# Kernel tuning notes

Hardware: AMD Instinct MI355X
Metric: run time of the kernel (lower is better)

## Reference

```python
import jax, jax.numpy as jnp
import numpy as np

B, P, C = 64, 196, 768   # batch, num_patches, hidden_size
HS = 384                 # hidden_s (token-mixing hidden dim)
NG = 8                   # num_grids
GMIN, GMAX = -1.0, 1.0


def _rbf(x):
    # fast-KAN radial basis: exp(-((x - grid_i)/denom)^2), grid over [GMIN, GMAX]
    grid = jnp.linspace(GMIN, GMAX, NG).astype(x.dtype)
    denom = (GMAX - GMIN) / (NG - 1)
    return jnp.exp(-jnp.square((x[..., None] - grid) / denom))  # [..., din, NG]


def _kan_linear(x, spline_w, base_w, base_b):
    # x: [..., din]; spline_w: [dout, din*NG]; base_w: [dout, din]; base_b: [dout]
    basis = _rbf(x).reshape(*x.shape[:-1], -1)          # [..., din*NG]
    out = basis @ spline_w.T                            # spline term (no bias)
    out = out + jax.nn.silu(x) @ base_w.T + base_b      # base update term
    return out


def setup_inputs() -> dict:
    key = jax.random.key(0)
    ks = jax.random.split(key, 5)
    s = 0.1  # spline_weight_init_scale
    return {
        "x": jax.random.normal(ks[0], (B, P, C), jnp.float32),
        "fc1_spline_w": jax.random.normal(ks[1], (HS, P * NG), jnp.float32) * (s / np.sqrt(P * NG)),
        "fc1_base_w": jax.random.normal(ks[2], (HS, P), jnp.float32) / np.sqrt(P),
        "fc1_base_b": jnp.zeros((HS,), jnp.float32),
        "fc2_spline_w": jax.random.normal(ks[3], (P, HS * NG), jnp.float32) * (s / np.sqrt(HS * NG)),
        "fc2_base_w": jax.random.normal(ks[4], (P, HS), jnp.float32) / np.sqrt(HS),
        "fc2_base_b": jnp.zeros((P,), jnp.float32),
    }


def reference(x, fc1_spline_w, fc1_base_w, fc1_base_b,
              fc2_spline_w, fc2_base_w, fc2_base_b):
    skip_param = 1.0
    # token mixing: permute so KANLinear acts over the patch axis
    h = jnp.swapaxes(x, 1, 2)                                   # [B, C, P]
    h = _kan_linear(h, fc1_spline_w, fc1_base_w, fc1_base_b)    # [B, C, HS]
    # dropout p=0 -> identity; the two intermediate permutes cancel
    h = _kan_linear(h, fc2_spline_w, fc2_base_w, fc2_base_b)    # [B, C, P]
    out = jnp.swapaxes(h, 1, 2)                                 # [B, P, C]
    return out + skip_param * x
```

## Files before the change

### kernel.cpp

```cpp
#include <hip/hip_runtime.h>
#include <cstdint>

#define B_  64
#define P_  196
#define C_  768
#define HS_ 384
#define M_  49152
#define RT_ 96
#define NB_ (M_ / RT_)

#define NC1 13
#define KT1 111
#define NT1 12
#define NC2 24
#define KT2 216
#define NT2 7

#define H1_ELEMS  ((size_t)M_ * HS_)
#define W1P_ELEMS ((size_t)KT1 * NT1 * 512)
#define W2P_ELEMS ((size_t)KT2 * NT2 * 512)

typedef __attribute__((ext_vector_type(8)))  short short8;
typedef __attribute__((ext_vector_type(16))) float f32x16;

#define MFMA(w, a, c) __builtin_amdgcn_mfma_f32_32x32x16_bf16((w), (a), (c), 0, 0, 0)

static __device__ __forceinline__ float bf2f(unsigned short u) {
    union { unsigned int i; float f; } v; v.i = ((unsigned int)u) << 16; return v.f;
}
static __device__ __forceinline__ unsigned short f2bf_rne(float f) {
    union { float f; unsigned int i; } v; v.f = f;
    unsigned int r = v.i + 0x7FFFu + ((v.i >> 16) & 1u);
    return (unsigned short)(r >> 16);
}
static __device__ __forceinline__ unsigned int pack2(float a, float b) {
    unsigned int ua = __float_as_uint(a) + 0x8000u;
    unsigned int ub = __float_as_uint(b) + 0x8000u;
    return __builtin_amdgcn_perm(ub, ua, 0x07060302u);
}
static __device__ __forceinline__ short8 rbf8(float s) {
    const float Rr = 1.2011224087864498f;
    const float Aa = 4.2039284307525743f;
    float t1 = __builtin_fmaf(Aa, s, Aa);
    union { short8 s8; unsigned int u[4]; } r;
#pragma unroll
    for (int q = 0; q < 4; q++) {
        float u0 = t1 - (float)(2 * q) * Rr;
        float u1 = t1 - (float)(2 * q + 1) * Rr;
        r.u[q] = pack2(__builtin_amdgcn_exp2f(-u0 * u0),
                       __builtin_amdgcn_exp2f(-u1 * u1));
    }
    return r.s8;
}
static __device__ __forceinline__ unsigned int silu2(float a, float b) {
    const float L2E = 1.4426950408889634f;
    float fa = a * __builtin_amdgcn_rcpf(1.f + __builtin_amdgcn_exp2f(-L2E * a));
    float fb = b * __builtin_amdgcn_rcpf(1.f + __builtin_amdgcn_exp2f(-L2E * b));
    return pack2(fa, fb);
}

static __device__ __forceinline__ void block_sync_lds() {
    __builtin_amdgcn_sched_barrier(0);
    asm volatile("s_waitcnt lgkmcnt(0)" ::: "memory");
    __builtin_amdgcn_s_barrier();
    __builtin_amdgcn_sched_barrier(0);
}

__global__ void pack_w_kernel(const float* __restrict__ w1s,
                              const float* __restrict__ w1b,
                              const float* __restrict__ w2s,
                              const float* __restrict__ w2b,
                              unsigned short* __restrict__ w1p,
                              unsigned short* __restrict__ w2p) {
    size_t idx = (size_t)blockIdx.x * 256 + threadIdx.x;
    if (idx < W1P_ELEMS) {
        int j    = idx & 7;
        int lane = (idx >> 3) & 63;
        int lin  = idx >> 9;
        int nt   = lin % NT1;
        int tt   = lin / NT1;
        int cc   = (tt < 108) ? tt / 9 : 12;
        int kk   = (tt < 108) ? tt % 9 : (tt - 108);
        int ktl  = (cc < 12) ? kk : ((kk < 2) ? kk : 8);
        int n = nt * 32 + (lane & 31);
        int khalf = lane >> 5;
        float v = 0.f;
        if (ktl < 8) {
            int p = cc * 16 + ktl * 2 + khalf;
            if (p < P_) v = w1s[(size_t)n * 1568 + p * 8 + j];
        } else {
            int p = cc * 16 + khalf * 8 + j;
            if (p < P_) v = w1b[(size_t)n * 196 + p];
        }
        w1p[idx] = f2bf_rne(v);
    } else {
        size_t idx2 = idx - W1P_ELEMS;
        if (idx2 < W2P_ELEMS) {
            int j    = idx2 & 7;
            int lane = (idx2 >> 3) & 63;
            int lin  = idx2 >> 9;
            int nt   = lin % NT2;
            int tt   = lin / NT2;
            int cc   = tt / 9;
            int ktl  = tt % 9;
            int n = nt * 32 + (lane & 31);
            int khalf = lane >> 5;
            float v = 0.f;
            if (n < P_) {
                if (ktl < 8) {
                    int s = cc * 16 + ktl * 2 + khalf;
                    v = w2s[(size_t)n * 3072 + s * 8 + j];
                } else {
                    int s = cc * 16 + khalf * 8 + j;
                    v = w2b[(size_t)n * 384 + s];
                }
            }
            w2p[idx2] = f2bf_rne(v);
        }
    }
}

#define TS_  1536
#define FB_  (9 * TS_)


__global__ __launch_bounds__(256, 2)
void fc1_kernel(const float* __restrict__ x,
                const unsigned short* __restrict__ w1p,
                const float* __restrict__ b1,
                unsigned short* __restrict__ h1t) {
    __shared__ __align__(16) unsigned short frag[2 * FB_];
    int blk = blockIdx.x;
    int tid = threadIdx.x;
    int b   = blk >> 3;
    int c0  = (blk & 7) * RT_;
    const float* xb = x + (size_t)b * (P_ * C_);

    int colA = tid & 63, scA = tid >> 6;
    int colB = 64 + (tid & 31), scB = tid >> 5;
    int pbase_rbfA  = ((colA >> 5) << 9) + (colA & 31) * 8;
    int pbase_rbfB  = 1024 + (colB & 31) * 8;
    int pbase_siluA = 8 * TS_ + ((colA >> 5) << 9) + ((scA >> 1) << 8) + (colA & 31) * 8 + (scA & 1) * 4;
    int pbase_siluB = 8 * TS_ + 1024 + ((scB >> 2) << 8) + (colB & 31) * 8 + (scB & 3) * 2;

    int wave = tid >> 6, lane = tid & 63;
    int l31 = lane & 31, half = lane >> 5;
    int nt0 = wave * 3;

    f32x16 acc[3][3];
#pragma unroll
    for (int rt = 0; rt < 3; rt++)
#pragma unroll
        for (int nt = 0; nt < 3; nt++)
#pragma unroll
            for (int i = 0; i < 16; i++) acc[rt][nt][i] = 0.f;

    const short8* wp = (const short8*)w1p;
    short8 wbuf[2][3];

    auto wload = [&](int d, const short8* wt0, int kk) {
        const short8* wt = wt0 + (size_t)kk * (NT1 * 64);
        wbuf[d][0] = wt[0]; wbuf[d][1] = wt[64]; wbuf[d][2] = wt[128];
    };
    auto do_mfma = [&](short8 w0, short8 w1, short8 w2,
                       short8 a0, short8 a1, short8 a2) {
        acc[0][0] = MFMA(w0, a0, acc[0][0]); acc[1][0] = MFMA(w0, a1, acc[1][0]); acc[2][0] = MFMA(w0, a2, acc[2][0]);
        acc[0][1] = MFMA(w1, a0, acc[0][1]); acc[1][1] = MFMA(w1, a1, acc[1][1]); acc[2][1] = MFMA(w1, a2, acc[2][1]);
        acc[0][2] = MFMA(w2, a0, acc[0][2]); acc[1][2] = MFMA(w2, a1, acc[1][2]); acc[2][2] = MFMA(w2, a2, acc[2][2]);
    };
    auto produce = [&](int fb, const float (&ra)[4], const float (&rb2)[2]) {
#pragma unroll
        for (int i = 0; i < 4; i++) {
            int sl = scA * 4 + i;
            *(short8*)&frag[fb + (sl >> 1) * TS_ + ((sl & 1) << 8) + pbase_rbfA] = rbf8(ra[i]);
        }
#pragma unroll
        for (int i = 0; i < 2; i++) {
            int sl = scB * 2 + i;
            *(short8*)&frag[fb + (sl >> 1) * TS_ + ((sl & 1) << 8) + pbase_rbfB] = rbf8(rb2[i]);
        }
        uint2 sv;
        sv.x = silu2(ra[0], ra[1]);
        sv.y = silu2(ra[2], ra[3]);
        *(uint2*)&frag[fb + pbase_siluA] = sv;
        *(unsigned int*)&frag[fb + pbase_siluB] = silu2(rb2[0], rb2[1]);
    };
    auto body = [&](int cc, const float (&rbPA)[4], const float (&rbPB)[2],
                    float (&rbLA)[4], float (&rbLB)[2]) {
        const short8* wt0 = wp + ((size_t)(cc * 9) * NT1 + nt0) * 64 + lane;
        wload(0, wt0, 0); wload(1, wt0, 1);
        int fbP = ((cc + 1) & 1) * FB_;
        const unsigned short* fg = &frag[(cc & 1) * FB_];
        short8 a0 = *(const short8*)&fg[lane * 8];
        short8 a1 = *(const short8*)&fg[512 + lane * 8];
        short8 a2 = *(const short8*)&fg[1024 + lane * 8];
#pragma unroll
        for (int kk = 0; kk < 9; kk++) {
            short8 na0, na1, na2;
            if (kk < 8) {
                na0 = *(const short8*)&fg[(kk + 1) * TS_ + lane * 8];
                na1 = *(const short8*)&fg[(kk + 1) * TS_ + 512 + lane * 8];
                na2 = *(const short8*)&fg[(kk + 1) * TS_ + 1024 + lane * 8];
            }
            short8 w0 = wbuf[kk & 1][0], w1 = wbuf[kk & 1][1], w2 = wbuf[kk & 1][2];
            if (kk < 7) wload(kk & 1, wt0, kk + 2);
            if (kk < 4) {
                int sl = scA * 4 + kk;
                *(short8*)&frag[fbP + (sl >> 1) * TS_ + ((sl & 1) << 8) + pbase_rbfA] = rbf8(rbPA[kk]);
            } else if (kk == 4) {
#pragma unroll
                for (int i = 0; i < 2; i++) {
                    int sl = scB * 2 + i;
                    *(short8*)&frag[fbP + (sl >> 1) * TS_ + ((sl & 1) << 8) + pbase_rbfB] = rbf8(rbPB[i]);
                }
            } else if (kk == 5) {
                uint2 sv;
                sv.x = silu2(rbPA[0], rbPA[1]);
                sv.y = silu2(rbPA[2], rbPA[3]);
                *(uint2*)&frag[fbP + pbase_siluA] = sv;
                *(unsigned int*)&frag[fbP + pbase_siluB] = silu2(rbPB[0], rbPB[1]);
            } else if (kk == 6) {
#pragma unroll
                for (int i = 0; i < 2; i++) {
                    int p = (cc + 2) * 16 + scA * 4 + i;
                    p = (p < P_) ? p : (P_ - 1);
                    rbLA[i] = xb[(size_t)p * C_ + c0 + colA];
                }
            } else if (kk == 7) {
#pragma unroll
                for (int i = 2; i < 4; i++) {
                    int p = (cc + 2) * 16 + scA * 4 + i;
                    p = (p < P_) ? p : (P_ - 1);
                    rbLA[i] = xb[(size_t)p * C_ + c0 + colA];
                }
            } else {
#pragma unroll
                for (int i = 0; i < 2; i++) {
                    int p = (cc + 2) * 16 + scB * 2 + i;
                    p = (p < P_) ? p : (P_ - 1);
                    rbLB[i] = xb[(size_t)p * C_ + c0 + colB];
                }
            }
            do_mfma(w0, w1, w2, a0, a1, a2);
            if (kk < 8) { a0 = na0; a1 = na1; a2 = na2; }
        }
        block_sync_lds();
    };

    float rbA_A[4], rbB_A[4], rbA_B[2], rbB_B[2];
#pragma unroll
    for (int i = 0; i < 4; i++) {
        rbA_A[i] = xb[(size_t)(scA * 4 + i) * C_ + c0 + colA];
        rbB_A[i] = xb[(size_t)(16 + scA * 4 + i) * C_ + c0 + colA];
    }
#pragma unroll
    for (int i = 0; i < 2; i++) {
        rbA_B[i] = xb[(size_t)(scB * 2 + i) * C_ + c0 + colB];
        rbB_B[i] = xb[(size_t)(16 + scB * 2 + i) * C_ + c0 + colB];
    }
    produce(0, rbA_A, rbA_B);
    block_sync_lds();

    for (int c2 = 0; c2 < 6; c2++) {
        body(2 * c2,     rbB_A, rbB_B, rbA_A, rbA_B);
        body(2 * c2 + 1, rbA_A, rbA_B, rbB_A, rbB_B);
    }
    {
        const short8* wt0 = wp + ((size_t)108 * NT1 + nt0) * 64 + lane;
        wload(0, wt0, 0); wload(1, wt0, 1);
        const unsigned short* fg = &frag[0];
#pragma unroll
        for (int kk = 0; kk < 3; kk++) {
            short8 w0 = wbuf[kk & 1][0], w1 = wbuf[kk & 1][1], w2 = wbuf[kk & 1][2];
            if (kk == 0) wload(0, wt0, 2);
            int ktl = (kk < 2) ? kk : 8;
            short8 a0 = *(const short8*)&fg[ktl * TS_ + lane * 8];
            short8 a1 = *(const short8*)&fg[ktl * TS_ + 512 + lane * 8];
            short8 a2 = *(const short8*)&fg[ktl * TS_ + 1024 + lane * 8];
            do_mfma(w0, w1, w2, a0, a1, a2);
        }
    }

#pragma unroll
    for (int nt = 0; nt < 3; nt++) {
        int n0 = (nt0 + nt) * 32 + 4 * half;
#pragma unroll
        for (int reg = 0; reg < 16; reg++) {
            int n = n0 + (reg & 3) + 8 * (reg >> 2);
            float bv = b1[n];
#pragma unroll
            for (int rt = 0; rt < 3; rt++) {
                h1t[(size_t)n * M_ + blk * RT_ + rt * 32 + l31] = f2bf_rne(acc[rt][nt][reg] + bv);
            }
        }
    }
}

__global__ __launch_bounds__(256, 2)
void fc2_kernel(const unsigned short* __restrict__ h1t,
                const unsigned short* __restrict__ w2p,
                const float* __restrict__ b2,
                const float* __restrict__ x,
                float* __restrict__ out) {
    __shared__ __align__(16) unsigned short frag[2 * FB_];
    int blk = blockIdx.x;
    int tid = threadIdx.x;
    int rbase = blk * RT_;

    int colA = tid & 63, scA = tid >> 6;
    int colB = 64 + (tid & 31), scB = tid >> 5;
    int pbase_rbfA  = ((colA >> 5) << 9) + (colA & 31) * 8;
    int pbase_rbfB  = 1024 + (colB & 31) * 8;
    int pbase_siluA = 8 * TS_ + ((colA >> 5) << 9) + ((scA >> 1) << 8) + (colA & 31) * 8 + (scA & 1) * 4;
    int pbase_siluB = 8 * TS_ + 1024 + ((scB >> 2) << 8) + (colB & 31) * 8 + (scB & 3) * 2;

    int wave = tid >> 6, lane = tid & 63;
    int l31 = lane & 31, half = lane >> 5;
    int nt0 = wave * 2;
    int ntn = (wave < 3) ? 2 : 1;
    int off1 = (ntn > 1) ? 64 : 0;

    f32x16 acc[3][2];
#pragma unroll
    for (int rt = 0; rt < 3; rt++)
#pragma unroll
        for (int nt = 0; nt < 2; nt++)
#pragma unroll
            for (int i = 0; i < 16; i++) acc[rt][nt][i] = 0.f;

    const short8* wp = (const short8*)w2p;
    short8 wbuf[2][2];

    auto wload = [&](int d, const short8* wt0, int kk) {
        const short8* wt = wt0 + (size_t)kk * (NT2 * 64);
        wbuf[d][0] = wt[0]; wbuf[d][1] = wt[off1];
    };
    auto do_mfma = [&](short8 w0, short8 w1, short8 a0, short8 a1, short8 a2) {
        acc[0][0] = MFMA(w0, a0, acc[0][0]); acc[1][0] = MFMA(w0, a1, acc[1][0]); acc[2][0] = MFMA(w0, a2, acc[2][0]);
        if (ntn == 2) {
            acc[0][1] = MFMA(w1, a0, acc[0][1]); acc[1][1] = MFMA(w1, a1, acc[1][1]); acc[2][1] = MFMA(w1, a2, acc[2][1]);
        }
    };
    auto produce = [&](int fb, const unsigned short (&ra)[4], const unsigned short (&rb2)[2]) {
        float v0 = bf2f(ra[0]), v1 = bf2f(ra[1]), v2 = bf2f(ra[2]), v3 = bf2f(ra[3]);
        float u0 = bf2f(rb2[0]), u1 = bf2f(rb2[1]);
        float vv[4] = {v0, v1, v2, v3};
#pragma unroll
        for (int i = 0; i < 4; i++) {
            int sl = scA * 4 + i;
            *(short8*)&frag[fb + (sl >> 1) * TS_ + ((sl & 1) << 8) + pbase_rbfA] = rbf8(vv[i]);
        }
        float uu[2] = {u0, u1};
#pragma unroll
        for (int i = 0; i < 2; i++) {
            int sl = scB * 2 + i;
            *(short8*)&frag[fb + (sl >> 1) * TS_ + ((sl & 1) << 8) + pbase_rbfB] = rbf8(uu[i]);
        }
        uint2 sv;
        sv.x = silu2(v0, v1);
        sv.y = silu2(v2, v3);
        *(uint2*)&frag[fb + pbase_siluA] = sv;
        *(unsigned int*)&frag[fb + pbase_siluB] = silu2(u0, u1);
    };
    auto body = [&](int cc, const unsigned short (&rbPA)[4], const unsigned short (&rbPB)[2],
                    unsigned short (&rbLA)[4], unsigned short (&rbLB)[2]) {
        bool doProd = (cc + 1 < NC2);
        const short8* wt0 = wp + ((size_t)(cc * 9) * NT2 + nt0) * 64 + lane;
        wload(0, wt0, 0); wload(1, wt0, 1);
        int fbP = ((cc + 1) & 1) * FB_;
        const unsigned short* fg = &frag[(cc & 1) * FB_];
        short8 a0 = *(const short8*)&fg[lane * 8];
        short8 a1 = *(const short8*)&fg[512 + lane * 8];
        short8 a2 = *(const short8*)&fg[1024 + lane * 8];
#pragma unroll
        for (int kk = 0; kk < 9; kk++) {
            short8 na0, na1, na2;
            if (kk < 8) {
                na0 = *(const short8*)&fg[(kk + 1) * TS_ + lane * 8];
                na1 = *(const short8*)&fg[(kk + 1) * TS_ + 512 + lane * 8];
                na2 = *(const short8*)&fg[(kk + 1) * TS_ + 1024 + lane * 8];
            }
            short8 w0 = wbuf[kk & 1][0], w1 = wbuf[kk & 1][1];
            if (kk < 7) wload(kk & 1, wt0, kk + 2);
            if (kk < 4) {
                if (doProd) {
                    int sl = scA * 4 + kk;
                    *(short8*)&frag[fbP + (sl >> 1) * TS_ + ((sl & 1) << 8) + pbase_rbfA] =
                        rbf8(bf2f(rbPA[kk]));
                }
            } else if (kk == 4) {
                if (doProd) {
#pragma unroll
                    for (int i = 0; i < 2; i++) {
                        int sl = scB * 2 + i;
                        *(short8*)&frag[fbP + (sl >> 1) * TS_ + ((sl & 1) << 8) + pbase_rbfB] =
                            rbf8(bf2f(rbPB[i]));
                    }
                }
            } else if (kk == 5) {
                if (doProd) {
                    uint2 sv;
                    sv.x = silu2(bf2f(rbPA[0]), bf2f(rbPA[1]));
                    sv.y = silu2(bf2f(rbPA[2]), bf2f(rbPA[3]));
                    *(uint2*)&frag[fbP + pbase_siluA] = sv;
                    *(unsigned int*)&frag[fbP + pbase_siluB] = silu2(bf2f(rbPB[0]), bf2f(rbPB[1]));
                }
            } else if (kk == 6) {
#pragma unroll
                for (int i = 0; i < 2; i++) {
                    int s = (cc + 2) * 16 + scA * 4 + i;
                    s = (s < HS_) ? s : (HS_ - 1);
                    rbLA[i] = h1t[(size_t)s * M_ + rbase + colA];
                }
            } else if (kk == 7) {
#pragma unroll
                for (int i = 2; i < 4; i++) {
                    int s = (cc + 2) * 16 + scA * 4 + i;
                    s = (s < HS_) ? s : (HS_ - 1);
                    rbLA[i] = h1t[(size_t)s * M_ + rbase + colA];
                }
            } else {
#pragma unroll
                for (int i = 0; i < 2; i++) {
                    int s = (cc + 2) * 16 + scB * 2 + i;
                    s = (s < HS_) ? s : (HS_ - 1);
                    rbLB[i] = h1t[(size_t)s * M_ + rbase + colB];
                }
            }
            do_mfma(w0, w1, a0, a1, a2);
            if (kk < 8) { a0 = na0; a1 = na1; a2 = na2; }
        }
        block_sync_lds();
    };

    unsigned short rbA_A[4], rbB_A[4], rbA_B[2], rbB_B[2];
#pragma unroll
    for (int i = 0; i < 4; i++) {
        rbA_A[i] = h1t[(size_t)(scA * 4 + i) * M_ + rbase + colA];
        rbB_A[i] = h1t[(size_t)(16 + scA * 4 + i) * M_ + rbase + colA];
    }
#pragma unroll
    for (int i = 0; i < 2; i++) {
        rbA_B[i] = h1t[(size_t)(scB * 2 + i) * M_ + rbase + colB];
        rbB_B[i] = h1t[(size_t)(16 + scB * 2 + i) * M_ + rbase + colB];
    }
    produce(0, rbA_A, rbA_B);
    block_sync_lds();

    for (int c2 = 0; c2 < 12; c2++) {
        body(2 * c2,     rbB_A, rbB_B, rbA_A, rbA_B);
        body(2 * c2 + 1, rbA_A, rbA_B, rbB_A, rbB_B);
    }

    int b = blk >> 3;
    int c0 = (blk & 7) * RT_;
#pragma unroll
    for (int nt = 0; nt < 2; nt++) {
        if (nt < ntn) {
            int p0 = (nt0 + nt) * 32 + 4 * half;
#pragma unroll
            for (int reg = 0; reg < 16; reg++) {
                int p = p0 + (reg & 3) + 8 * (reg >> 2);
                if (p < P_) {
                    float bv = b2[p];
#pragma unroll
                    for (int rt = 0; rt < 3; rt++) {
                        size_t off = ((size_t)b * P_ + p) * C_ + c0 + rt * 32 + l31;
                        out[off] = acc[rt][nt][reg] + bv + x[off];
                    }
                }
            }
        }
    }
}

extern "C" void kernel_launch(void* const* d_in, const int* in_sizes, int n_in,
                              void* d_out, int out_size, void* d_ws, size_t ws_size,
                              hipStream_t stream) {
    const float* x   = (const float*)d_in[0];
    const float* w1s = (const float*)d_in[1];
    const float* w1b = (const float*)d_in[2];
    const float* b1  = (const float*)d_in[3];
    const float* w2s = (const float*)d_in[4];
    const float* w2b = (const float*)d_in[5];
    const float* b2  = (const float*)d_in[6];
    float* out = (float*)d_out;

    unsigned short* h1t = (unsigned short*)d_ws;
    unsigned short* w1p = h1t + H1_ELEMS;
    unsigned short* w2p = w1p + W1P_ELEMS;

    int pack_blocks = (int)((W1P_ELEMS + W2P_ELEMS) / 256);
    pack_w_kernel<<<pack_blocks, 256, 0, stream>>>(w1s, w1b, w2s, w2b, w1p, w2p);
    fc1_kernel<<<NB_, 256, 0, stream>>>(x, w1p, b1, h1t);
    fc2_kernel<<<NB_, 256, 0, stream>>>(h1t, w2p, b2, x, out);
}
```

Before: 243.4 us.

## Warp-specialize fc1/fc2 into producer waves and MFMA consumer waves

Both GEMM kernels now launch 512 threads. Four producer waves load inputs and compute RBF and SiLU fragments into a 4-deep LDS ring, and four consumer waves, raised in priority, only load weights and issue MFMAs. This moves basis computation and global loads out of the MFMA loop so they overlap with matrix work. In exchange, LDS use doubles and occupancy drops to one block per CU, with one block-wide barrier per pair of chunks.

```diff
diff --git a/kernel.cpp b/kernel.cpp
--- a/kernel.cpp
+++ b/kernel.cpp
@@ -123,27 +123,78 @@
 #define TS_  1536
 #define FB_  (9 * TS_)
 
-
-__global__ __launch_bounds__(256, 2)
+__global__ __launch_bounds__(512, 1)
 void fc1_kernel(const float* __restrict__ x,
                 const unsigned short* __restrict__ w1p,
                 const float* __restrict__ b1,
                 unsigned short* __restrict__ h1t) {
-    __shared__ __align__(16) unsigned short frag[2 * FB_];
+    __shared__ __align__(16) unsigned short frag[4 * FB_];
     int blk = blockIdx.x;
     int tid = threadIdx.x;
     int b   = blk >> 3;
     int c0  = (blk & 7) * RT_;
     const float* xb = x + (size_t)b * (P_ * C_);
-
-    int colA = tid & 63, scA = tid >> 6;
-    int colB = 64 + (tid & 31), scB = tid >> 5;
-    int pbase_rbfA  = ((colA >> 5) << 9) + (colA & 31) * 8;
-    int pbase_rbfB  = 1024 + (colB & 31) * 8;
-    int pbase_siluA = 8 * TS_ + ((colA >> 5) << 9) + ((scA >> 1) << 8) + (colA & 31) * 8 + (scA & 1) * 4;
-    int pbase_siluB = 8 * TS_ + 1024 + ((scB >> 2) << 8) + (colB & 31) * 8 + (scB & 3) * 2;
-
-    int wave = tid >> 6, lane = tid & 63;
+    int wave = tid >> 6;
+
+    if (wave >= 4) {
+        int ptid = tid & 255;
+        int colA = ptid & 63, scA = ptid >> 6;
+        int colB = 64 + (ptid & 31), scB = ptid >> 5;
+        int pbase_rbfA  = ((colA >> 5) << 9) + (colA & 31) * 8;
+        int pbase_rbfB  = 1024 + (colB & 31) * 8;
+        int pbase_siluA = 8 * TS_ + ((colA >> 5) << 9) + ((scA >> 1) << 8) + (colA & 31) * 8 + (scA & 1) * 4;
+        int pbase_siluB = 8 * TS_ + 1024 + ((scB >> 2) << 8) + (colB & 31) * 8 + (scB & 3) * 2;
+
+        auto loadc = [&](int cc, float (&va)[4], float (&vb)[2]) {
+#pragma unroll
+            for (int i = 0; i < 4; i++) {
+                int p = cc * 16 + scA * 4 + i; p = (p < P_) ? p : (P_ - 1);
+                va[i] = xb[(size_t)p * C_ + c0 + colA];
+            }
+#pragma unroll
+            for (int i = 0; i < 2; i++) {
+                int p = cc * 16 + scB * 2 + i; p = (p < P_) ? p : (P_ - 1);
+                vb[i] = xb[(size_t)p * C_ + c0 + colB];
+            }
+        };
+        auto produce = [&](int cc, const float (&ra)[4], const float (&rb2)[2]) {
+            int fb = (cc & 3) * FB_;
+#pragma unroll
+            for (int i = 0; i < 4; i++) {
+                int sl = scA * 4 + i;
+                *(short8*)&frag[fb + (sl >> 1) * TS_ + ((sl & 1) << 8) + pbase_rbfA] = rbf8(ra[i]);
+            }
+#pragma unroll
+            for (int i = 0; i < 2; i++) {
+                int sl = scB * 2 + i;
+                *(short8*)&frag[fb + (sl >> 1) * TS_ + ((sl & 1) << 8) + pbase_rbfB] = rbf8(rb2[i]);
+            }
+            uint2 sv;
+            sv.x = silu2(ra[0], ra[1]);
+            sv.y = silu2(ra[2], ra[3]);
+            *(uint2*)&frag[fb + pbase_siluA] = sv;
+            *(unsigned int*)&frag[fb + pbase_siluB] = silu2(rb2[0], rb2[1]);
+        };
+
+        float vA[4], uA[2], vB[4], uB[2];
+        loadc(0, vA, uA); loadc(1, vB, uB);
+        produce(0, vA, uA); produce(1, vB, uB);
+        loadc(2, vA, uA); loadc(3, vB, uB);
+        block_sync_lds();
+        for (int t = 0; t < 7; t++) {
+            int cP = 2 * t + 2;
+            if (cP     < NC1) produce(cP,     vA, uA);
+            if (cP + 1 < NC1) produce(cP + 1, vB, uB);
+            int n0 = (cP + 2 < NC1) ? cP + 2 : NC1 - 1;
+            int n1 = (cP + 3 < NC1) ? cP + 3 : NC1 - 1;
+            loadc(n0, vA, uA); loadc(n1, vB, uB);
+            block_sync_lds();
+        }
+        return;
+    }
+
+    __builtin_amdgcn_s_setprio(1);
+    int lane = tid & 63;
     int l31 = lane & 31, half = lane >> 5;
     int nt0 = wave * 3;
 
@@ -158,6 +209,7 @@
     const short8* wp = (const short8*)w1p;
     short8 wbuf[2][3];
 
+    auto wt0_of = [&](int cc) { return wp + ((size_t)(cc * 9) * NT1 + nt0) * 64 + lane; };
     auto wload = [&](int d, const short8* wt0, int kk) {
         const short8* wt = wt0 + (size_t)kk * (NT1 * 64);
         wbuf[d][0] = wt[0]; wbuf[d][1] = wt[64]; wbuf[d][2] = wt[128];
@@ -168,29 +220,8 @@
         acc[0][1] = MFMA(w1, a0, acc[0][1]); acc[1][1] = MFMA(w1, a1, acc[1][1]); acc[2][1] = MFMA(w1, a2, acc[2][1]);
         acc[0][2] = MFMA(w2, a0, acc[0][2]); acc[1][2] = MFMA(w2, a1, acc[1][2]); acc[2][2] = MFMA(w2, a2, acc[2][2]);
     };
-    auto produce = [&](int fb, const float (&ra)[4], const float (&rb2)[2]) {
-#pragma unroll
-        for (int i = 0; i < 4; i++) {
-            int sl = scA * 4 + i;
-            *(short8*)&frag[fb + (sl >> 1) * TS_ + ((sl & 1) << 8) + pbase_rbfA] = rbf8(ra[i]);
-        }
-#pragma unroll
-        for (int i = 0; i < 2; i++) {
-            int sl = scB * 2 + i;
-            *(short8*)&frag[fb + (sl >> 1) * TS_ + ((sl & 1) << 8) + pbase_rbfB] = rbf8(rb2[i]);
-        }
-        uint2 sv;
-        sv.x = silu2(ra[0], ra[1]);
-        sv.y = silu2(ra[2], ra[3]);
-        *(uint2*)&frag[fb + pbase_siluA] = sv;
-        *(unsigned int*)&frag[fb + pbase_siluB] = silu2(rb2[0], rb2[1]);
-    };
-    auto body = [&](int cc, const float (&rbPA)[4], const float (&rbPB)[2],
-                    float (&rbLA)[4], float (&rbLB)[2]) {
-        const short8* wt0 = wp + ((size_t)(cc * 9) * NT1 + nt0) * 64 + lane;
-        wload(0, wt0, 0); wload(1, wt0, 1);
-        int fbP = ((cc + 1) & 1) * FB_;
-        const unsigned short* fg = &frag[(cc & 1) * FB_];
+    auto consume = [&](int cc, const short8* wt0) {
+        const unsigned short* fg = &frag[(cc & 3) * FB_];
         short8 a0 = *(const short8*)&fg[lane * 8];
         short8 a1 = *(const short8*)&fg[512 + lane * 8];
         short8 a2 = *(const short8*)&fg[1024 + lane * 8];
@@ -204,81 +235,39 @@
             }
             short8 w0 = wbuf[kk & 1][0], w1 = wbuf[kk & 1][1], w2 = wbuf[kk & 1][2];
             if (kk < 7) wload(kk & 1, wt0, kk + 2);
-            if (kk < 4) {
-                int sl = scA * 4 + kk;
-                *(short8*)&frag[fbP + (sl >> 1) * TS_ + ((sl & 1) << 8) + pbase_rbfA] = rbf8(rbPA[kk]);
-            } else if (kk == 4) {
-#pragma unroll
-                for (int i = 0; i < 2; i++) {
-                    int sl = scB * 2 + i;
-                    *(short8*)&frag[fbP + (sl >> 1) * TS_ + ((sl & 1) << 8) + pbase_rbfB] = rbf8(rbPB[i]);
-                }
-            } else if (kk == 5) {
-                uint2 sv;
-                sv.x = silu2(rbPA[0], rbPA[1]);
-                sv.y = silu2(rbPA[2], rbPA[3]);
-                *(uint2*)&frag[fbP + pbase_siluA] = sv;
-                *(unsigned int*)&frag[fbP + pbase_siluB] = silu2(rbPB[0], rbPB[1]);
-            } else if (kk == 6) {
-#pragma unroll
-                for (int i = 0; i < 2; i++) {
-                    int p = (cc + 2) * 16 + scA * 4 + i;
-                    p = (p < P_) ? p : (P_ - 1);
-                    rbLA[i] = xb[(size_t)p * C_ + c0 + colA];
-                }
-            } else if (kk == 7) {
-#pragma unroll
-                for (int i = 2; i < 4; i++) {
-                    int p = (cc + 2) * 16 + scA * 4 + i;
-                    p = (p < P_) ? p : (P_ - 1);
-                    rbLA[i] = xb[(size_t)p * C_ + c0 + colA];
-                }
-            } else {
-#pragma unroll
-                for (int i = 0; i < 2; i++) {
-                    int p = (cc + 2) * 16 + scB * 2 + i;
-                    p = (p < P_) ? p : (P_ - 1);
-                    rbLB[i] = xb[(size_t)p * C_ + c0 + colB];
-                }
-            }
             do_mfma(w0, w1, w2, a0, a1, a2);
             if (kk < 8) { a0 = na0; a1 = na1; a2 = na2; }
         }
+    };
+
+    const short8* wtP = wt0_of(0);
+    wload(0, wtP, 0); wload(1, wtP, 1);
+    block_sync_lds();
+    for (int t = 0; t < 7; t++) {
+        if (t < 6) {
+            consume(2 * t, wtP);
+            const short8* wtQ = wt0_of(2 * t + 1);
+            wload(0, wtQ, 0); wload(1, wtQ, 1);
+            consume(2 * t + 1, wtQ);
+            wtP = wt0_of(2 * t + 2);
+            wload(0, wtP, 0); wload(1, wtP, 1);
+        } else {
+            const unsigned short* fg = &frag[(12 & 3) * FB_];
+            short8 a0 = *(const short8*)&fg[lane * 8];
+            short8 a1 = *(const short8*)&fg[512 + lane * 8];
+            short8 a2 = *(const short8*)&fg[1024 + lane * 8];
+            short8 c0v = *(const short8*)&fg[TS_ + lane * 8];
+            short8 c1v = *(const short8*)&fg[TS_ + 512 + lane * 8];
+            short8 c2v = *(const short8*)&fg[TS_ + 1024 + lane * 8];
+            short8 s0 = *(const short8*)&fg[8 * TS_ + lane * 8];
+            short8 s1 = *(const short8*)&fg[8 * TS_ + 512 + lane * 8];
+            short8 s2 = *(const short8*)&fg[8 * TS_ + 1024 + lane * 8];
+            do_mfma(wbuf[0][0], wbuf[0][1], wbuf[0][2], a0, a1, a2);
+            wload(0, wtP, 2);
+            do_mfma(wbuf[1][0], wbuf[1][1], wbuf[1][2], c0v, c1v, c2v);
+            do_mfma(wbuf[0][0], wbuf[0][1], wbuf[0][2], s0, s1, s2);
+        }
         block_sync_lds();
-    };
-
-    float rbA_A[4], rbB_A[4], rbA_B[2], rbB_B[2];
-#pragma unroll
-    for (int i = 0; i < 4; i++) {
-        rbA_A[i] = xb[(size_t)(scA * 4 + i) * C_ + c0 + colA];
-        rbB_A[i] = xb[(size_t)(16 + scA * 4 + i) * C_ + c0 + colA];
-    }
-#pragma unroll
-    for (int i = 0; i < 2; i++) {
-        rbA_B[i] = xb[(size_t)(scB * 2 + i) * C_ + c0 + colB];
-        rbB_B[i] = xb[(size_t)(16 + scB * 2 + i) * C_ + c0 + colB];
-    }
-    produce(0, rbA_A, rbA_B);
-    block_sync_lds();
-
-    for (int c2 = 0; c2 < 6; c2++) {
-        body(2 * c2,     rbB_A, rbB_B, rbA_A, rbA_B);
-        body(2 * c2 + 1, rbA_A, rbA_B, rbB_A, rbB_B);
-    }
-    {
-        const short8* wt0 = wp + ((size_t)108 * NT1 + nt0) * 64 + lane;
-        wload(0, wt0, 0); wload(1, wt0, 1);
-        const unsigned short* fg = &frag[0];
-#pragma unroll
-        for (int kk = 0; kk < 3; kk++) {
-            short8 w0 = wbuf[kk & 1][0], w1 = wbuf[kk & 1][1], w2 = wbuf[kk & 1][2];
-            if (kk == 0) wload(0, wt0, 2);
-            int ktl = (kk < 2) ? kk : 8;
-            short8 a0 = *(const short8*)&fg[ktl * TS_ + lane * 8];
-            short8 a1 = *(const short8*)&fg[ktl * TS_ + 512 + lane * 8];
-            short8 a2 = *(const short8*)&fg[ktl * TS_ + 1024 + lane * 8];
-            do_mfma(w0, w1, w2, a0, a1, a2);
-        }
     }
 
 #pragma unroll
@@ -296,25 +285,81 @@
     }
 }
 
-__global__ __launch_bounds__(256, 2)
+__global__ __launch_bounds__(512, 1)
 void fc2_kernel(const unsigned short* __restrict__ h1t,
                 const unsigned short* __restrict__ w2p,
                 const float* __restrict__ b2,
                 const float* __restrict__ x,
                 float* __restrict__ out) {
-    __shared__ __align__(16) unsigned short frag[2 * FB_];
+    __shared__ __align__(16) unsigned short frag[4 * FB_];
     int blk = blockIdx.x;
     int tid = threadIdx.x;
     int rbase = blk * RT_;
-
-    int colA = tid & 63, scA = tid >> 6;
-    int colB = 64 + (tid & 31), scB = tid >> 5;
-    int pbase_rbfA  = ((colA >> 5) << 9) + (colA & 31) * 8;
-    int pbase_rbfB  = 1024 + (colB & 31) * 8;
-    int pbase_siluA = 8 * TS_ + ((colA >> 5) << 9) + ((scA >> 1) << 8) + (colA & 31) * 8 + (scA & 1) * 4;
-    int pbase_siluB = 8 * TS_ + 1024 + ((scB >> 2) << 8) + (colB & 31) * 8 + (scB & 3) * 2;
-
-    int wave = tid >> 6, lane = tid & 63;
+    int wave = tid >> 6;
+
+    if (wave >= 4) {
+        int ptid = tid & 255;
+        int colA = ptid & 63, scA = ptid >> 6;
+        int colB = 64 + (ptid & 31), scB = ptid >> 5;
+        int pbase_rbfA  = ((colA >> 5) << 9) + (colA & 31) * 8;
+        int pbase_rbfB  = 1024 + (colB & 31) * 8;
+        int pbase_siluA = 8 * TS_ + ((colA >> 5) << 9) + ((scA >> 1) << 8) + (colA & 31) * 8 + (scA & 1) * 4;
+        int pbase_siluB = 8 * TS_ + 1024 + ((scB >> 2) << 8) + (colB & 31) * 8 + (scB & 3) * 2;
+
+        auto loadc = [&](int cc, unsigned short (&va)[4], unsigned short (&vb)[2]) {
+#pragma unroll
+            for (int i = 0; i < 4; i++) {
+                int s = cc * 16 + scA * 4 + i; s = (s < HS_) ? s : (HS_ - 1);
+                va[i] = h1t[(size_t)s * M_ + rbase + colA];
+            }
+#pragma unroll
+            for (int i = 0; i < 2; i++) {
+                int s = cc * 16 + scB * 2 + i; s = (s < HS_) ? s : (HS_ - 1);
+                vb[i] = h1t[(size_t)s * M_ + rbase + colB];
+            }
+        };
+        auto produce = [&](int cc, const unsigned short (&ra)[4], const unsigned short (&rb2)[2]) {
+            int fb = (cc & 3) * FB_;
+            float v0 = bf2f(ra[0]), v1 = bf2f(ra[1]), v2 = bf2f(ra[2]), v3 = bf2f(ra[3]);
+            float u0 = bf2f(rb2[0]), u1 = bf2f(rb2[1]);
+            float vv[4] = {v0, v1, v2, v3};
+#pragma unroll
+            for (int i = 0; i < 4; i++) {
+                int sl = scA * 4 + i;
+                *(short8*)&frag[fb + (sl >> 1) * TS_ + ((sl & 1) << 8) + pbase_rbfA] = rbf8(vv[i]);
+            }
+            float uu[2] = {u0, u1};
+#pragma unroll
+            for (int i = 0; i < 2; i++) {
+                int sl = scB * 2 + i;
+                *(short8*)&frag[fb + (sl >> 1) * TS_ + ((sl & 1) << 8) + pbase_rbfB] = rbf8(uu[i]);
+            }
+            uint2 sv;
+            sv.x = silu2(v0, v1);
+            sv.y = silu2(v2, v3);
+            *(uint2*)&frag[fb + pbase_siluA] = sv;
+            *(unsigned int*)&frag[fb + pbase_siluB] = silu2(u0, u1);
+        };
+
+        unsigned short vA[4], uA[2], vB[4], uB[2];
+        loadc(0, vA, uA); loadc(1, vB, uB);
+        produce(0, vA, uA); produce(1, vB, uB);
+        loadc(2, vA, uA); loadc(3, vB, uB);
+        block_sync_lds();
+        for (int t = 0; t < 12; t++) {
+            int cP = 2 * t + 2;
+            if (cP     < NC2) produce(cP,     vA, uA);
+            if (cP + 1 < NC2) produce(cP + 1, vB, uB);
+            int n0 = (cP + 2 < NC2) ? cP + 2 : NC2 - 1;
+            int n1 = (cP + 3 < NC2) ? cP + 3 : NC2 - 1;
+            loadc(n0, vA, uA); loadc(n1, vB, uB);
+            block_sync_lds();
+        }
+        return;
+    }
+
+    __builtin_amdgcn_s_setprio(1);
+    int lane = tid & 63;
     int l31 = lane & 31, half = lane >> 5;
     int nt0 = wave * 2;
     int ntn = (wave < 3) ? 2 : 1;
@@ -331,6 +376,7 @@
     const short8* wp = (const short8*)w2p;
     short8 wbuf[2][2];
 
+    auto wt0_of = [&](int cc) { return wp + ((size_t)(cc * 9) * NT2 + nt0) * 64 + lane; };
     auto wload = [&](int d, const short8* wt0, int kk) {
         const short8* wt = wt0 + (size_t)kk * (NT2 * 64);
         wbuf[d][0] = wt[0]; wbuf[d][1] = wt[off1];
@@ -341,34 +387,8 @@
             acc[0][1] = MFMA(w1, a0, acc[0][1]); acc[1][1] = MFMA(w1, a1, acc[1][1]); acc[2][1] = MFMA(w1, a2, acc[2][1]);
         }
     };
-    auto produce = [&](int fb, const unsigned short (&ra)[4], const unsigned short (&rb2)[2]) {
-        float v0 = bf2f(ra[0]), v1 = bf2f(ra[1]), v2 = bf2f(ra[2]), v3 = bf2f(ra[3]);
-        float u0 = bf2f(rb2[0]), u1 = bf2f(rb2[1]);
-        float vv[4] = {v0, v1, v2, v3};
-#pragma unroll
-        for (int i = 0; i < 4; i++) {
-            int sl = scA * 4 + i;
-            *(short8*)&frag[fb + (sl >> 1) * TS_ + ((sl & 1) << 8) + pbase_rbfA] = rbf8(vv[i]);
-        }
-        float uu[2] = {u0, u1};
-#pragma unroll
-        for (int i = 0; i < 2; i++) {
-            int sl = scB * 2 + i;
-            *(short8*)&frag[fb + (sl >> 1) * TS_ + ((sl & 1) << 8) + pbase_rbfB] = rbf8(uu[i]);
-        }
-        uint2 sv;
-        sv.x = silu2(v0, v1);
-        sv.y = silu2(v2, v3);
-        *(uint2*)&frag[fb + pbase_siluA] = sv;
-        *(unsigned int*)&frag[fb + pbase_siluB] = silu2(u0, u1);
-    };
-    auto body = [&](int cc, const unsigned short (&rbPA)[4], const unsigned short (&rbPB)[2],
-                    unsigned short (&rbLA)[4], unsigned short (&rbLB)[2]) {
-        bool doProd = (cc + 1 < NC2);
-        const short8* wt0 = wp + ((size_t)(cc * 9) * NT2 + nt0) * 64 + lane;
-        wload(0, wt0, 0); wload(1, wt0, 1);
-        int fbP = ((cc + 1) & 1) * FB_;
-        const unsigned short* fg = &frag[(cc & 1) * FB_];
+    auto consume = [&](int cc, const short8* wt0) {
+        const unsigned short* fg = &frag[(cc & 3) * FB_];
         short8 a0 = *(const short8*)&fg[lane * 8];
         short8 a1 = *(const short8*)&fg[512 + lane * 8];
         short8 a2 = *(const short8*)&fg[1024 + lane * 8];
@@ -382,74 +402,23 @@
             }
             short8 w0 = wbuf[kk & 1][0], w1 = wbuf[kk & 1][1];
             if (kk < 7) wload(kk & 1, wt0, kk + 2);
-            if (kk < 4) {
-                if (doProd) {
-                    int sl = scA * 4 + kk;
-                    *(short8*)&frag[fbP + (sl >> 1) * TS_ + ((sl & 1) << 8) + pbase_rbfA] =
-                        rbf8(bf2f(rbPA[kk]));
-                }
-            } else if (kk == 4) {
-                if (doProd) {
-#pragma unroll
-                    for (int i = 0; i < 2; i++) {
-                        int sl = scB * 2 + i;
-                        *(short8*)&frag[fbP + (sl >> 1) * TS_ + ((sl & 1) << 8) + pbase_rbfB] =
-                            rbf8(bf2f(rbPB[i]));
-                    }
-                }
-            } else if (kk == 5) {
-                if (doProd) {
-                    uint2 sv;
-                    sv.x = silu2(bf2f(rbPA[0]), bf2f(rbPA[1]));
-                    sv.y = silu2(bf2f(rbPA[2]), bf2f(rbPA[3]));
-                    *(uint2*)&frag[fbP + pbase_siluA] = sv;
-                    *(unsigned int*)&frag[fbP + pbase_siluB] = silu2(bf2f(rbPB[0]), bf2f(rbPB[1]));
-                }
-            } else if (kk == 6) {
-#pragma unroll
-                for (int i = 0; i < 2; i++) {
-                    int s = (cc + 2) * 16 + scA * 4 + i;
-                    s = (s < HS_) ? s : (HS_ - 1);
-                    rbLA[i] = h1t[(size_t)s * M_ + rbase + colA];
-                }
-            } else if (kk == 7) {
-#pragma unroll
-                for (int i = 2; i < 4; i++) {
-                    int s = (cc + 2) * 16 + scA * 4 + i;
-                    s = (s < HS_) ? s : (HS_ - 1);
-                    rbLA[i] = h1t[(size_t)s * M_ + rbase + colA];
-                }
-            } else {
-#pragma unroll
-                for (int i = 0; i < 2; i++) {
-                    int s = (cc + 2) * 16 + scB * 2 + i;
-                    s = (s < HS_) ? s : (HS_ - 1);
-                    rbLB[i] = h1t[(size_t)s * M_ + rbase + colB];
-                }
-            }
             do_mfma(w0, w1, a0, a1, a2);
             if (kk < 8) { a0 = na0; a1 = na1; a2 = na2; }
         }
+    };
+
+    const short8* wtP = wt0_of(0);
+    wload(0, wtP, 0); wload(1, wtP, 1);
+    block_sync_lds();
+    for (int t = 0; t < 12; t++) {
+        consume(2 * t, wtP);
+        const short8* wtQ = wt0_of(2 * t + 1);
+        wload(0, wtQ, 0); wload(1, wtQ, 1);
+        consume(2 * t + 1, wtQ);
+        int nc = (2 * t + 2 < NC2) ? 2 * t + 2 : NC2 - 1;
+        wtP = wt0_of(nc);
+        wload(0, wtP, 0); wload(1, wtP, 1);
         block_sync_lds();
-    };
-
-    unsigned short rbA_A[4], rbB_A[4], rbA_B[2], rbB_B[2];
-#pragma unroll
-    for (int i = 0; i < 4; i++) {
-        rbA_A[i] = h1t[(size_t)(scA * 4 + i) * M_ + rbase + colA];
-        rbB_A[i] = h1t[(size_t)(16 + scA * 4 + i) * M_ + rbase + colA];
-    }
-#pragma unroll
-    for (int i = 0; i < 2; i++) {
-        rbA_B[i] = h1t[(size_t)(scB * 2 + i) * M_ + rbase + colB];
-        rbB_B[i] = h1t[(size_t)(16 + scB * 2 + i) * M_ + rbase + colB];
-    }
-    produce(0, rbA_A, rbA_B);
-    block_sync_lds();
-
-    for (int c2 = 0; c2 < 12; c2++) {
-        body(2 * c2,     rbB_A, rbB_B, rbA_A, rbA_B);
-        body(2 * c2 + 1, rbA_A, rbA_B, rbB_A, rbB_B);
     }
 
     int b = blk >> 3;
@@ -492,6 +461,6 @@
 
     int pack_blocks = (int)((W1P_ELEMS + W2P_ELEMS) / 256);
     pack_w_kernel<<<pack_blocks, 256, 0, stream>>>(w1s, w1b, w2s, w2b, w1p, w2p);
-    fc1_kernel<<<NB_, 256, 0, stream>>>(x, w1p, b1, h1t);
-    fc2_kernel<<<NB_, 256, 0, stream>>>(h1t, w2p, b2, x, out);
-}
+    fc1_kernel<<<NB_, 512, 0, stream>>>(x, w1p, b1, h1t);
+    fc2_kernel<<<NB_, 512, 0, stream>>>(h1t, w2p, b2, x, out);
+}
```

Measured after the change: 291.2 us. 1.2x slower.

## Restructure fc2 inner loop into three phases with batched loads and setprio MFMA bursts

Applied to the files above, without the earlier changes.

Replaces the per-k software-pipelined loop in the fc2 kernel (next fragment and weight prefetched one step ahead) with three phases per chunk. Each phase first loads three k-steps of A fragments from LDS and weights from global, does its share of producer and global-load work, then runs a block barrier and a burst of MFMAs under raised wave priority. The intent is to group memory and compute so waves on a CU interleave MFMA bursts better. In exchange it adds three barriers per chunk instead of one, removes the one-step-ahead register prefetch so global weight-load latency is exposed before each burst, and raises register pressure from the larger fragment and weight buffers.

```diff
diff --git a/kernel.cpp b/kernel.cpp
--- a/kernel.cpp
+++ b/kernel.cpp
@@ -123,7 +123,6 @@
 #define TS_  1536
 #define FB_  (9 * TS_)
 
-
 __global__ __launch_bounds__(256, 2)
 void fc1_kernel(const float* __restrict__ x,
                 const unsigned short* __restrict__ w1p,
@@ -329,18 +328,9 @@
             for (int i = 0; i < 16; i++) acc[rt][nt][i] = 0.f;
 
     const short8* wp = (const short8*)w2p;
-    short8 wbuf[2][2];
-
-    auto wload = [&](int d, const short8* wt0, int kk) {
-        const short8* wt = wt0 + (size_t)kk * (NT2 * 64);
-        wbuf[d][0] = wt[0]; wbuf[d][1] = wt[off1];
-    };
-    auto do_mfma = [&](short8 w0, short8 w1, short8 a0, short8 a1, short8 a2) {
-        acc[0][0] = MFMA(w0, a0, acc[0][0]); acc[1][0] = MFMA(w0, a1, acc[1][0]); acc[2][0] = MFMA(w0, a2, acc[2][0]);
-        if (ntn == 2) {
-            acc[0][1] = MFMA(w1, a0, acc[0][1]); acc[1][1] = MFMA(w1, a1, acc[1][1]); acc[2][1] = MFMA(w1, a2, acc[2][1]);
-        }
-    };
+    short8 wbuf[3][2];
+    short8 af[3][3];
+
     auto produce = [&](int fb, const unsigned short (&ra)[4], const unsigned short (&rb2)[2]) {
         float v0 = bf2f(ra[0]), v1 = bf2f(ra[1]), v2 = bf2f(ra[2]), v3 = bf2f(ra[3]);
         float u0 = bf2f(rb2[0]), u1 = bf2f(rb2[1]);
@@ -362,33 +352,56 @@
         *(uint2*)&frag[fb + pbase_siluA] = sv;
         *(unsigned int*)&frag[fb + pbase_siluB] = silu2(u0, u1);
     };
+
     auto body = [&](int cc, const unsigned short (&rbPA)[4], const unsigned short (&rbPB)[2],
                     unsigned short (&rbLA)[4], unsigned short (&rbLB)[2]) {
         bool doProd = (cc + 1 < NC2);
-        const short8* wt0 = wp + ((size_t)(cc * 9) * NT2 + nt0) * 64 + lane;
-        wload(0, wt0, 0); wload(1, wt0, 1);
+        const unsigned short* fg = &frag[(cc & 1) * FB_];
         int fbP = ((cc + 1) & 1) * FB_;
-        const unsigned short* fg = &frag[(cc & 1) * FB_];
-        short8 a0 = *(const short8*)&fg[lane * 8];
-        short8 a1 = *(const short8*)&fg[512 + lane * 8];
-        short8 a2 = *(const short8*)&fg[1024 + lane * 8];
-#pragma unroll
-        for (int kk = 0; kk < 9; kk++) {
-            short8 na0, na1, na2;
-            if (kk < 8) {
-                na0 = *(const short8*)&fg[(kk + 1) * TS_ + lane * 8];
-                na1 = *(const short8*)&fg[(kk + 1) * TS_ + 512 + lane * 8];
-                na2 = *(const short8*)&fg[(kk + 1) * TS_ + 1024 + lane * 8];
-            }
-            short8 w0 = wbuf[kk & 1][0], w1 = wbuf[kk & 1][1];
-            if (kk < 7) wload(kk & 1, wt0, kk + 2);
-            if (kk < 4) {
+#pragma unroll
+        for (int p = 0; p < 3; p++) {
+#pragma unroll
+            for (int k = 0; k < 3; k++) {
+                int t = 3 * p + k;
+                af[k][0] = *(const short8*)&fg[t * TS_ + lane * 8];
+                af[k][1] = *(const short8*)&fg[t * TS_ + 512 + lane * 8];
+                af[k][2] = *(const short8*)&fg[t * TS_ + 1024 + lane * 8];
+            }
+            const short8* wt0 = wp + ((size_t)(cc * 9 + 3 * p) * NT2 + nt0) * 64 + lane;
+#pragma unroll
+            for (int k = 0; k < 3; k++) {
+                const short8* wt = wt0 + (size_t)k * (NT2 * 64);
+                wbuf[k][0] = wt[0]; wbuf[k][1] = wt[off1];
+            }
+            if (p == 0) {
                 if (doProd) {
-                    int sl = scA * 4 + kk;
-                    *(short8*)&frag[fbP + (sl >> 1) * TS_ + ((sl & 1) << 8) + pbase_rbfA] =
-                        rbf8(bf2f(rbPA[kk]));
-                }
-            } else if (kk == 4) {
+#pragma unroll
+                    for (int i = 0; i < 2; i++) {
+                        int sl = scA * 4 + i;
+                        *(short8*)&frag[fbP + (sl >> 1) * TS_ + ((sl & 1) << 8) + pbase_rbfA] =
+                            rbf8(bf2f(rbPA[i]));
+                    }
+                }
+#pragma unroll
+                for (int i = 0; i < 2; i++) {
+                    int s = (cc + 2) * 16 + scA * 4 + i; s = (s < HS_) ? s : (HS_ - 1);
+                    rbLA[i] = h1t[(size_t)s * M_ + rbase + colA];
+                }
+            } else if (p == 1) {
+                if (doProd) {
+#pragma unroll
+                    for (int i = 2; i < 4; i++) {
+                        int sl = scA * 4 + i;
+                        *(short8*)&frag[fbP + (sl >> 1) * TS_ + ((sl & 1) << 8) + pbase_rbfA] =
+                            rbf8(bf2f(rbPA[i]));
+                    }
+                }
+#pragma unroll
+                for (int i = 2; i < 4; i++) {
+                    int s = (cc + 2) * 16 + scA * 4 + i; s = (s < HS_) ? s : (HS_ - 1);
+                    rbLA[i] = h1t[(size_t)s * M_ + rbase + colA];
+                }
+            } else {
                 if (doProd) {
 #pragma unroll
                     for (int i = 0; i < 2; i++) {
@@ -396,41 +409,34 @@
                         *(short8*)&frag[fbP + (sl >> 1) * TS_ + ((sl & 1) << 8) + pbase_rbfB] =
                             rbf8(bf2f(rbPB[i]));
                     }
-                }
-            } else if (kk == 5) {
-                if (doProd) {
                     uint2 sv;
                     sv.x = silu2(bf2f(rbPA[0]), bf2f(rbPA[1]));
                     sv.y = silu2(bf2f(rbPA[2]), bf2f(rbPA[3]));
                     *(uint2*)&frag[fbP + pbase_siluA] = sv;
                     *(unsigned int*)&frag[fbP + pbase_siluB] = silu2(bf2f(rbPB[0]), bf2f(rbPB[1]));
                 }
-            } else if (kk == 6) {
 #pragma unroll
                 for (int i = 0; i < 2; i++) {
-                    int s = (cc + 2) * 16 + scA * 4 + i;
-                    s = (s < HS_) ? s : (HS_ - 1);
-                    rbLA[i] = h1t[(size_t)s * M_ + rbase + colA];
-                }
-            } else if (kk == 7) {
-#pragma unroll
-                for (int i = 2; i < 4; i++) {
-                    int s = (cc + 2) * 16 + scA * 4 + i;
-                    s = (s < HS_) ? s : (HS_ - 1);
-                    rbLA[i] = h1t[(size_t)s * M_ + rbase + colA];
-                }
-            } else {
-#pragma unroll
-                for (int i = 0; i < 2; i++) {
-                    int s = (cc + 2) * 16 + scB * 2 + i;
-                    s = (s < HS_) ? s : (HS_ - 1);
+                    int s = (cc + 2) * 16 + scB * 2 + i; s = (s < HS_) ? s : (HS_ - 1);
                     rbLB[i] = h1t[(size_t)s * M_ + rbase + colB];
                 }
             }
-            do_mfma(w0, w1, a0, a1, a2);
-            if (kk < 8) { a0 = na0; a1 = na1; a2 = na2; }
-        }
-        block_sync_lds();
+            block_sync_lds();
+            __builtin_amdgcn_s_setprio(1);
+#pragma unroll
+            for (int k = 0; k < 3; k++) {
+                short8 w0 = wbuf[k][0], w1 = wbuf[k][1];
+                acc[0][0] = MFMA(w0, af[k][0], acc[0][0]);
+                acc[1][0] = MFMA(w0, af[k][1], acc[1][0]);
+                acc[2][0] = MFMA(w0, af[k][2], acc[2][0]);
+                if (ntn == 2) {
+                    acc[0][1] = MFMA(w1, af[k][0], acc[0][1]);
+                    acc[1][1] = MFMA(w1, af[k][1], acc[1][1]);
+                    acc[2][1] = MFMA(w1, af[k][2], acc[2][1]);
+                }
+            }
+            __builtin_amdgcn_s_setprio(0);
+        }
     };
 
     unsigned short rbA_A[4], rbB_A[4], rbA_B[2], rbB_B[2];
```

Result: no change. 245.3 us (+0.8%).
